# Performance work log

Hardware: AMD Instinct MI355X
Metric: run time of the kernel (lower is better)

The kernel has to match this reference:

```python
import jax, jax.numpy as jnp
import numpy as np

N_NODES = 100000
IN_CH = 256
OUT_CH = 128
HID = 2 * OUT_CH  # 256
N_EDGES = 1600000


def gcn_conv(x, src, dst, W, b, num_nodes):
    """PyG GCNConv: add self-loops, symmetric deg^-1/2 normalization,
    linear transform, scatter-add aggregation, plus bias."""
    h = x @ W  # [N, F_out]
    loop = jnp.arange(num_nodes, dtype=src.dtype)
    src_f = jnp.concatenate([src, loop])
    dst_f = jnp.concatenate([dst, loop])
    ones = jnp.ones(src_f.shape[0], dtype=h.dtype)
    deg = jax.ops.segment_sum(ones, dst_f, num_segments=num_nodes)
    dis = jnp.where(deg > 0, jax.lax.rsqrt(deg), 0.0)
    norm = dis[src_f] * dis[dst_f]  # [E+N]
    msg = h[src_f] * norm[:, None]  # [E+N, F_out]
    out = jax.ops.segment_sum(msg, dst_f, num_segments=num_nodes)
    return out + b


def setup_inputs() -> dict:
    key = jax.random.key(0)
    ks = jax.random.split(key, 8)
    x = jax.random.normal(ks[0], (N_NODES, IN_CH), dtype=jnp.float32)
    edge_index = jax.random.randint(ks[1], (2, N_EDGES), 0, N_NODES, dtype=jnp.int64 if jax.config.jax_enable_x64 else jnp.int32)
    s1 = 1.0 / np.sqrt(IN_CH)
    s2 = 1.0 / np.sqrt(HID)
    W1 = jax.random.uniform(ks[2], (IN_CH, HID), jnp.float32, -s1, s1)
    b1 = jnp.zeros((HID,), jnp.float32)
    W_mu = jax.random.uniform(ks[3], (HID, OUT_CH), jnp.float32, -s2, s2)
    b_mu = jnp.zeros((OUT_CH,), jnp.float32)
    W_lv = jax.random.uniform(ks[4], (HID, OUT_CH), jnp.float32, -s2, s2)
    b_lv = jnp.zeros((OUT_CH,), jnp.float32)
    return {"x": x, "edge_index": edge_index, "W1": W1, "b1": b1,
            "W_mu": W_mu, "b_mu": b_mu, "W_lv": W_lv, "b_lv": b_lv}


def reference(x, edge_index, W1, b1, W_mu, b_mu, W_lv, b_lv):
    src, dst = edge_index[0], edge_index[1]
    h = jax.nn.relu(gcn_conv(x, src, dst, W1, b1, N_NODES))
    mu = gcn_conv(h, src, dst, W_mu, b_mu, N_NODES)
    logvar = gcn_conv(h, src, dst, W_lv, b_lv, N_NODES)
    return (mu, logvar)
```

## Files before the change

kernel.cpp:

```cpp
#include <hip/hip_runtime.h>
#include <hip/hip_fp16.h>

#define N_NODES 100000
#define E_EDGES 1600000
#define F 256
#define LV_OFF 12800000
#define SCAN_BLK 98
#define GEMM_BLKS 1564
#define FILL_BLKS 6250

typedef _Float16 half8 __attribute__((ext_vector_type(8)));
typedef _Float16 f16x4 __attribute__((ext_vector_type(4)));
typedef float    f32x4 __attribute__((ext_vector_type(4)));

__global__ void k_zero(int* __restrict__ p, int n) {
    int i = blockIdx.x * 256 + threadIdx.x;
    if (i < n) p[i] = 0;
}

__global__ void k_count(const int* __restrict__ dst, int* __restrict__ cnt) {
    int e = blockIdx.x * 256 + threadIdx.x;
    if (e < E_EDGES) atomicAdd(&cnt[dst[e]], 1);
}

__global__ void k_dis(const int* __restrict__ cnt, float* __restrict__ dis) {
    int i = blockIdx.x * 256 + threadIdx.x;
    if (i < N_NODES) dis[i] = rsqrtf((float)cnt[i] + 1.0f);
}

__global__ __launch_bounds__(256) void k_scan1(const int* __restrict__ cnt,
                                               int* __restrict__ row_off,
                                               int* __restrict__ bsum) {
    __shared__ int sd[256];
    int tid = threadIdx.x;
    int base = blockIdx.x * 1024 + tid * 4;
    int c[4]; int s = 0;
#pragma unroll
    for (int k = 0; k < 4; k++) {
        int i = base + k;
        c[k] = (i < N_NODES) ? cnt[i] : 0;
        s += c[k];
    }
    sd[tid] = s;
    __syncthreads();
    for (int off = 1; off < 256; off <<= 1) {
        int t = (tid >= off) ? sd[tid - off] : 0;
        __syncthreads();
        sd[tid] += t;
        __syncthreads();
    }
    int run = sd[tid] - s;
#pragma unroll
    for (int k = 0; k < 4; k++) {
        int i = base + k;
        if (i < N_NODES) row_off[i] = run;
        run += c[k];
    }
    if (tid == 255) bsum[blockIdx.x] = sd[255];
}

__global__ void k_scan2(int* __restrict__ bsum) {
    if (threadIdx.x == 0 && blockIdx.x == 0) {
        int run = 0;
        for (int i = 0; i < SCAN_BLK; ++i) { int t = bsum[i]; bsum[i] = run; run += t; }
    }
}

__global__ __launch_bounds__(256) void k_scan3(int* __restrict__ row_off,
                                               const int* __restrict__ bsum,
                                               int* __restrict__ cursor) {
    int tid = threadIdx.x;
    int add = bsum[blockIdx.x];
    int base = blockIdx.x * 1024 + tid * 4;
#pragma unroll
    for (int k = 0; k < 4; k++) {
        int i = base + k;
        if (i < N_NODES) {
            int v = row_off[i] + add;
            row_off[i] = v;
            cursor[i] = v;
        }
    }
    if (blockIdx.x == 0 && tid == 0) row_off[N_NODES] = E_EDGES;
}

__global__ void k_wprep(const float* __restrict__ W1,
                        const float* __restrict__ Wmu, const float* __restrict__ Wlv,
                        _Float16* __restrict__ Wt1, _Float16* __restrict__ Wtc) {
    int idx = blockIdx.x * 256 + threadIdx.x;
    int n = idx >> 8, k = idx & 255;
    Wt1[n * 256 + k] = (_Float16)W1[k * 256 + n];
    float wc = (n < 128) ? Wmu[k * 128 + n] : Wlv[k * 128 + (n - 128)];
    Wtc[n * 256 + k] = (_Float16)wc;
}

__device__ __forceinline__ void gemm_tile(
    const float* __restrict__ A, const _Float16* __restrict__ Bt,
    const float* __restrict__ dis, _Float16* __restrict__ G, int M,
    int m0, int n0, int tid, _Float16* Ah, _Float16* Bh)
{
    const int wave = tid >> 6, lane = tid & 63;
    const int wm   = wave & 1, wn = wave >> 1;
    const int lrow = lane & 15, kgrp = lane >> 4;

    f32x4 acc[4][4];
#pragma unroll
    for (int i = 0; i < 4; i++)
#pragma unroll
        for (int j = 0; j < 4; j++) acc[i][j] = (f32x4){0.f, 0.f, 0.f, 0.f};

    const int sr = tid >> 4;
    const int kq = tid & 15;

    for (int kt = 0; kt < 256; kt += 64) {
#pragma unroll
        for (int p = 0; p < 8; ++p) {
            int row = p * 16 + sr;
            int gm = m0 + row; if (gm >= M) gm = M - 1;
            float4 v = *reinterpret_cast<const float4*>(A + (size_t)gm * F + kt + kq * 4);
            f16x4 h4;
            h4[0] = (_Float16)v.x; h4[1] = (_Float16)v.y;
            h4[2] = (_Float16)v.z; h4[3] = (_Float16)v.w;
            int sidx = row * 64 + ((kq * 4) ^ ((row & 7) << 3));
            *reinterpret_cast<f16x4*>(&Ah[sidx]) = h4;
        }
#pragma unroll
        for (int p = 0; p < 4; ++p) {
            int u = p * 256 + tid;
            int n = u >> 3, slot = u & 7;
            half8 hv = *reinterpret_cast<const half8*>(Bt + (size_t)(n0 + n) * F + kt + slot * 8);
            int sidx = n * 64 + ((slot * 8) ^ ((n & 7) << 3));
            *reinterpret_cast<half8*>(&Bh[sidx]) = hv;
        }
        __syncthreads();
#pragma unroll
        for (int ks = 0; ks < 2; ++ks) {
            int kk = ks * 32 + kgrp * 8;
            half8 ah[4], bh[4];
#pragma unroll
            for (int i = 0; i < 4; ++i) {
                int row = wm * 64 + i * 16 + lrow;
                ah[i] = *reinterpret_cast<const half8*>(&Ah[row * 64 + (kk ^ ((row & 7) << 3))]);
                int col = wn * 64 + i * 16 + lrow;
                bh[i] = *reinterpret_cast<const half8*>(&Bh[col * 64 + (kk ^ ((col & 7) << 3))]);
            }
#pragma unroll
            for (int i = 0; i < 4; ++i)
#pragma unroll
                for (int j = 0; j < 4; ++j)
                    acc[i][j] = __builtin_amdgcn_mfma_f32_16x16x32_f16(ah[i], bh[j], acc[i][j], 0, 0, 0);
        }
        __syncthreads();
    }

#pragma unroll
    for (int i = 0; i < 4; ++i) {
#pragma unroll
        for (int r = 0; r < 4; ++r) {
            int m = m0 + wm * 64 + i * 16 + kgrp * 4 + r;
            if (m >= M) continue;
            float dv = dis[m];
#pragma unroll
            for (int j = 0; j < 4; ++j) {
                int n = n0 + wn * 64 + j * 16 + lrow;
                G[(size_t)m * F + n] = (_Float16)(acc[i][j][r] * dv);
            }
        }
    }
}

__global__ __launch_bounds__(256) void k_gemm_fill(
    const float* __restrict__ A, const _Float16* __restrict__ Bt,
    const float* __restrict__ dis, _Float16* __restrict__ G, int M,
    const int* __restrict__ src, const int* __restrict__ dst,
    int* __restrict__ cursor, int* __restrict__ csr_src)
{
    __shared__ _Float16 Ah[128 * 64];
    __shared__ _Float16 Bh[128 * 64];
    int bid = blockIdx.x;
    int r5 = bid % 5;
    if (r5 == 0) {
        int gid = bid / 5;
        gemm_tile(A, Bt, dis, G, M, (gid >> 1) * 128, (gid & 1) * 128, threadIdx.x, Ah, Bh);
    } else {
        int fid = (bid / 5) * 4 + r5 - 1;
        int e = fid * 256 + threadIdx.x;
        if (e < E_EDGES) {
            int pos = atomicAdd(&cursor[dst[e]], 1);
            csr_src[pos] = src[e];
        }
    }
}

__global__ __launch_bounds__(256) void k_gemm_f16(
    const float* __restrict__ A, const _Float16* __restrict__ Bt,
    const float* __restrict__ dis, _Float16* __restrict__ G, int M)
{
    __shared__ _Float16 Ah[128 * 64];
    __shared__ _Float16 Bh[128 * 64];
    gemm_tile(A, Bt, dis, G, M, blockIdx.x * 128, blockIdx.y * 128, threadIdx.x, Ah, Bh);
}

__global__ __launch_bounds__(256) void k_aggregate_relu(
    const _Float16* __restrict__ g, const int* __restrict__ row_off,
    const int* __restrict__ csr_src, const float* __restrict__ dis,
    const float* __restrict__ b, float* __restrict__ h)
{
    int d = blockIdx.x * 4 + (threadIdx.x >> 6);
    int lane = threadIdx.x & 63;
    int hf = lane >> 5, lp = lane & 31;
    const half8* g8 = reinterpret_cast<const half8*>(g);
    float a[8] = {0,0,0,0,0,0,0,0}, a2[8] = {0,0,0,0,0,0,0,0};
    float a3[8] = {0,0,0,0,0,0,0,0}, a4[8] = {0,0,0,0,0,0,0,0};
    if (hf == 0) {
        half8 sv = g8[(size_t)d * 32 + lp];
#pragma unroll
        for (int k = 0; k < 8; k++) a[k] = (float)sv[k];
    }
    int j0 = row_off[d], j1 = row_off[d + 1];
    int j = j0 + hf;
    for (; j + 6 < j1; j += 8) {
        int s0 = csr_src[j], s1 = csr_src[j + 2], s2 = csr_src[j + 4], s3 = csr_src[j + 6];
        half8 v0 = g8[(size_t)s0 * 32 + lp];
        half8 v1 = g8[(size_t)s1 * 32 + lp];
        half8 v2 = g8[(size_t)s2 * 32 + lp];
        half8 v3 = g8[(size_t)s3 * 32 + lp];
#pragma unroll
        for (int k = 0; k < 8; k++) {
            a[k] += (float)v0[k]; a2[k] += (float)v1[k];
            a3[k] += (float)v2[k]; a4[k] += (float)v3[k];
        }
    }
    for (; j < j1; j += 2) {
        int s0 = csr_src[j];
        half8 v0 = g8[(size_t)s0 * 32 + lp];
#pragma unroll
        for (int k = 0; k < 8; k++) a[k] += (float)v0[k];
    }
#pragma unroll
    for (int k = 0; k < 8; k++) {
        a[k] += a2[k] + a3[k] + a4[k];
        a[k] += __shfl_xor(a[k], 32);
    }
    float sc = dis[d];
    int c = lp * 8 + hf * 4;
    float4 bb = *reinterpret_cast<const float4*>(b + c);
    float4 o;
    o.x = fmaxf(fmaf(sc, a[hf * 4 + 0], bb.x), 0.0f);
    o.y = fmaxf(fmaf(sc, a[hf * 4 + 1], bb.y), 0.0f);
    o.z = fmaxf(fmaf(sc, a[hf * 4 + 2], bb.z), 0.0f);
    o.w = fmaxf(fmaf(sc, a[hf * 4 + 3], bb.w), 0.0f);
    *reinterpret_cast<float4*>(h + (size_t)d * F + c) = o;
}

__global__ __launch_bounds__(256) void k_aggregate_out(
    const _Float16* __restrict__ g, const int* __restrict__ row_off,
    const int* __restrict__ csr_src, const float* __restrict__ dis,
    const float* __restrict__ bmu, const float* __restrict__ blv,
    float* __restrict__ out)
{
    int d = blockIdx.x * 4 + (threadIdx.x >> 6);
    int lane = threadIdx.x & 63;
    int hf = lane >> 5, lp = lane & 31;
    const half8* g8 = reinterpret_cast<const half8*>(g);
    float a[8] = {0,0,0,0,0,0,0,0}, a2[8] = {0,0,0,0,0,0,0,0};
    float a3[8] = {0,0,0,0,0,0,0,0}, a4[8] = {0,0,0,0,0,0,0,0};
    if (hf == 0) {
        half8 sv = g8[(size_t)d * 32 + lp];
#pragma unroll
        for (int k = 0; k < 8; k++) a[k] = (float)sv[k];
    }
    int j0 = row_off[d], j1 = row_off[d + 1];
    int j = j0 + hf;
    for (; j + 6 < j1; j += 8) {
        int s0 = csr_src[j], s1 = csr_src[j + 2], s2 = csr_src[j + 4], s3 = csr_src[j + 6];
        half8 v0 = g8[(size_t)s0 * 32 + lp];
        half8 v1 = g8[(size_t)s1 * 32 + lp];
        half8 v2 = g8[(size_t)s2 * 32 + lp];
        half8 v3 = g8[(size_t)s3 * 32 + lp];
#pragma unroll
        for (int k = 0; k < 8; k++) {
            a[k] += (float)v0[k]; a2[k] += (float)v1[k];
            a3[k] += (float)v2[k]; a4[k] += (float)v3[k];
        }
    }
    for (; j < j1; j += 2) {
        int s0 = csr_src[j];
        half8 v0 = g8[(size_t)s0 * 32 + lp];
#pragma unroll
        for (int k = 0; k < 8; k++) a[k] += (float)v0[k];
    }
#pragma unroll
    for (int k = 0; k < 8; k++) {
        a[k] += a2[k] + a3[k] + a4[k];
        a[k] += __shfl_xor(a[k], 32);
    }
    float sc = dis[d];
    int ch = lp * 8 + hf * 4;
    float va = a[hf * 4 + 0], vb = a[hf * 4 + 1], vc = a[hf * 4 + 2], vd = a[hf * 4 + 3];
    if (ch < 128) {
        float4 bb = *reinterpret_cast<const float4*>(bmu + ch);
        float4 o = make_float4(fmaf(sc, va, bb.x), fmaf(sc, vb, bb.y),
                               fmaf(sc, vc, bb.z), fmaf(sc, vd, bb.w));
        *reinterpret_cast<float4*>(out + (size_t)d * 128 + ch) = o;
    } else {
        int c2 = ch - 128;
        float4 bb = *reinterpret_cast<const float4*>(blv + c2);
        float4 o = make_float4(fmaf(sc, va, bb.x), fmaf(sc, vb, bb.y),
                               fmaf(sc, vc, bb.z), fmaf(sc, vd, bb.w));
        *reinterpret_cast<float4*>(out + LV_OFF + (size_t)d * 128 + c2) = o;
    }
}

extern "C" void kernel_launch(void* const* d_in, const int* in_sizes, int n_in,
                              void* d_out, int out_size, void* d_ws, size_t ws_size,
                              hipStream_t stream) {
    const float* x   = (const float*)d_in[0];
    const int*   ei  = (const int*)d_in[1];
    const int*   src = ei;
    const int*   dst = ei + E_EDGES;
    const float* W1  = (const float*)d_in[2];
    const float* b1  = (const float*)d_in[3];
    const float* Wmu = (const float*)d_in[4];
    const float* bmu = (const float*)d_in[5];
    const float* Wlv = (const float*)d_in[6];
    const float* blv = (const float*)d_in[7];
    float* out = (float*)d_out;

    char* ws = (char*)d_ws;
    size_t o = 0;
    auto carve = [&](size_t bytes) -> char* {
        char* p = ws + o;
        o = (o + bytes + 1023) & ~(size_t)1023;
        return p;
    };
    float*    dis     = (float*)   carve(400000);
    int*      cnt     = (int*)     carve(400000);
    int*      row_off = (int*)     carve(400004);
    int*      cursor  = (int*)     carve(400000);
    int*      bsum    = (int*)     carve(SCAN_BLK * 4);
    _Float16* Wt1     = (_Float16*)carve(131072);
    _Float16* Wtc     = (_Float16*)carve(131072);
    int*      csr_src = (int*)     carve((size_t)E_EDGES * 4);
    _Float16* g       = (_Float16*)carve((size_t)N_NODES * F * 2);
    (void)ws_size;

    k_zero <<<(N_NODES + 255) / 256, 256, 0, stream>>>(cnt, N_NODES);
    k_count<<<(E_EDGES + 255) / 256, 256, 0, stream>>>(dst, cnt);
    k_dis  <<<(N_NODES + 255) / 256, 256, 0, stream>>>(cnt, dis);
    k_scan1<<<SCAN_BLK, 256, 0, stream>>>(cnt, row_off, bsum);
    k_scan2<<<1, 64, 0, stream>>>(bsum);
    k_scan3<<<SCAN_BLK, 256, 0, stream>>>(row_off, bsum, cursor);
    k_wprep<<<256, 256, 0, stream>>>(W1, Wmu, Wlv, Wt1, Wtc);

    k_gemm_fill<<<5 * GEMM_BLKS, 256, 0, stream>>>(x, Wt1, dis, g, N_NODES,
                                                   src, dst, cursor, csr_src);
    k_aggregate_relu<<<N_NODES / 4, 256, 0, stream>>>(g, row_off, csr_src, dis, b1, out);

    dim3 gemm_grid(782, 2);
    k_gemm_f16<<<gemm_grid, 256, 0, stream>>>(out, Wtc, dis, g, N_NODES);
    k_aggregate_out<<<N_NODES / 4, 256, 0, stream>>>(g, row_off, csr_src, dis, bmu, blv, out);
}
```

Before: 515.6 us.

## Replace atomic CSR build with two-level bucket sort and widen GEMM tiles

Builds the CSR through a two-level binning scheme instead of global per-node atomics and a three-kernel scan. Edges are first bucketed by dst>>7 using shared-memory histograms, then sorted locally per bucket, and degrees and dis are derived inside the bucket pass. The GEMM now computes the full 256-wide output per block, which halves the A reloads, and the hidden layer is stored in fp16 so the second GEMM reads half the bytes. The cost is an extra 8-byte-per-edge intermediate buffer and one more pass over edges. The GEMM no longer overlaps with the CSR fill.

```diff
diff --git a/kernel.cpp b/kernel.cpp
--- a/kernel.cpp
+++ b/kernel.cpp
@@ -5,9 +5,9 @@
 #define E_EDGES 1600000
 #define F 256
 #define LV_OFF 12800000
-#define SCAN_BLK 98
-#define GEMM_BLKS 1564
-#define FILL_BLKS 6250
+#define NBUK 782
+#define EPB 8192
+#define NBLK_BIN 196
 
 typedef _Float16 half8 __attribute__((ext_vector_type(8)));
 typedef _Float16 f16x4 __attribute__((ext_vector_type(4)));
@@ -16,72 +16,6 @@
 __global__ void k_zero(int* __restrict__ p, int n) {
     int i = blockIdx.x * 256 + threadIdx.x;
     if (i < n) p[i] = 0;
-}
-
-__global__ void k_count(const int* __restrict__ dst, int* __restrict__ cnt) {
-    int e = blockIdx.x * 256 + threadIdx.x;
-    if (e < E_EDGES) atomicAdd(&cnt[dst[e]], 1);
-}
-
-__global__ void k_dis(const int* __restrict__ cnt, float* __restrict__ dis) {
-    int i = blockIdx.x * 256 + threadIdx.x;
-    if (i < N_NODES) dis[i] = rsqrtf((float)cnt[i] + 1.0f);
-}
-
-__global__ __launch_bounds__(256) void k_scan1(const int* __restrict__ cnt,
-                                               int* __restrict__ row_off,
-                                               int* __restrict__ bsum) {
-    __shared__ int sd[256];
-    int tid = threadIdx.x;
-    int base = blockIdx.x * 1024 + tid * 4;
-    int c[4]; int s = 0;
-#pragma unroll
-    for (int k = 0; k < 4; k++) {
-        int i = base + k;
-        c[k] = (i < N_NODES) ? cnt[i] : 0;
-        s += c[k];
-    }
-    sd[tid] = s;
-    __syncthreads();
-    for (int off = 1; off < 256; off <<= 1) {
-        int t = (tid >= off) ? sd[tid - off] : 0;
-        __syncthreads();
-        sd[tid] += t;
-        __syncthreads();
-    }
-    int run = sd[tid] - s;
-#pragma unroll
-    for (int k = 0; k < 4; k++) {
-        int i = base + k;
-        if (i < N_NODES) row_off[i] = run;
-        run += c[k];
-    }
-    if (tid == 255) bsum[blockIdx.x] = sd[255];
-}
-
-__global__ void k_scan2(int* __restrict__ bsum) {
-    if (threadIdx.x == 0 && blockIdx.x == 0) {
-        int run = 0;
-        for (int i = 0; i < SCAN_BLK; ++i) { int t = bsum[i]; bsum[i] = run; run += t; }
-    }
-}
-
-__global__ __launch_bounds__(256) void k_scan3(int* __restrict__ row_off,
-                                               const int* __restrict__ bsum,
-                                               int* __restrict__ cursor) {
-    int tid = threadIdx.x;
-    int add = bsum[blockIdx.x];
-    int base = blockIdx.x * 1024 + tid * 4;
-#pragma unroll
-    for (int k = 0; k < 4; k++) {
-        int i = base + k;
-        if (i < N_NODES) {
-            int v = row_off[i] + add;
-            row_off[i] = v;
-            cursor[i] = v;
-        }
-    }
-    if (blockIdx.x == 0 && tid == 0) row_off[N_NODES] = E_EDGES;
 }
 
 __global__ void k_wprep(const float* __restrict__ W1,
@@ -94,60 +28,167 @@
     Wtc[n * 256 + k] = (_Float16)wc;
 }
 
-__device__ __forceinline__ void gemm_tile(
-    const float* __restrict__ A, const _Float16* __restrict__ Bt,
-    const float* __restrict__ dis, _Float16* __restrict__ G, int M,
-    int m0, int n0, int tid, _Float16* Ah, _Float16* Bh)
+__global__ __launch_bounds__(256) void k_binA(const int* __restrict__ dst,
+                                              int* __restrict__ gcnt, int* __restrict__ cbase) {
+    __shared__ int h[NBUK];
+    int blk = blockIdx.x, tid = threadIdx.x;
+    for (int b = tid; b < NBUK; b += 256) h[b] = 0;
+    __syncthreads();
+    int e0 = blk * EPB, e1 = min(e0 + EPB, E_EDGES);
+    for (int e = e0 + tid; e < e1; e += 256) atomicAdd(&h[dst[e] >> 7], 1);
+    __syncthreads();
+    for (int b = tid; b < NBUK; b += 256) {
+        int c = h[b];
+        cbase[blk * NBUK + b] = c ? atomicAdd(&gcnt[b], c) : 0;
+    }
+}
+
+__global__ __launch_bounds__(1024) void k_scan782(const int* __restrict__ gcnt,
+                                                  int* __restrict__ gbase) {
+    __shared__ int sd[1024];
+    int tid = threadIdx.x;
+    int v = (tid < NBUK) ? gcnt[tid] : 0;
+    sd[tid] = v;
+    __syncthreads();
+    for (int off = 1; off < 1024; off <<= 1) {
+        int t = (tid >= off) ? sd[tid - off] : 0;
+        __syncthreads();
+        sd[tid] += t;
+        __syncthreads();
+    }
+    if (tid < NBUK) gbase[tid] = sd[tid] - v;
+    if (tid == NBUK - 1) gbase[NBUK] = sd[tid];
+}
+
+__global__ __launch_bounds__(256) void k_binC(const int* __restrict__ src, const int* __restrict__ dst,
+                                              const int* __restrict__ gbase, const int* __restrict__ cbase,
+                                              unsigned long long* __restrict__ ebuf) {
+    __shared__ int h2[NBUK];
+    __shared__ int bs[NBUK];
+    int blk = blockIdx.x, tid = threadIdx.x;
+    for (int b = tid; b < NBUK; b += 256) {
+        h2[b] = 0;
+        bs[b] = gbase[b] + cbase[blk * NBUK + b];
+    }
+    __syncthreads();
+    int e0 = blk * EPB, e1 = min(e0 + EPB, E_EDGES);
+    for (int e = e0 + tid; e < e1; e += 256) {
+        int d = dst[e];
+        int b = d >> 7;
+        int lr = atomicAdd(&h2[b], 1);
+        ebuf[bs[b] + lr] = ((unsigned long long)(unsigned)d << 32) | (unsigned)src[e];
+    }
+}
+
+__global__ __launch_bounds__(256) void k_binD(const unsigned long long* __restrict__ ebuf,
+                                              const int* __restrict__ gbase,
+                                              int* __restrict__ csr_src, int* __restrict__ row_off,
+                                              float* __restrict__ dis) {
+    __shared__ int dh[128], dsc[128], dcur[128];
+    int b = blockIdx.x, tid = threadIdx.x;
+    if (tid < 128) dh[tid] = 0;
+    __syncthreads();
+    int s0 = gbase[b], s1 = gbase[b + 1];
+    for (int i = s0 + tid; i < s1; i += 256)
+        atomicAdd(&dh[(int)(ebuf[i] >> 32) & 127], 1);
+    __syncthreads();
+    if (tid < 128) dsc[tid] = dh[tid];
+    __syncthreads();
+    for (int off = 1; off < 128; off <<= 1) {
+        int t = 0;
+        if (tid < 128 && tid >= off) t = dsc[tid - off];
+        __syncthreads();
+        if (tid < 128) dsc[tid] += t;
+        __syncthreads();
+    }
+    if (tid < 128) {
+        int ex = dsc[tid] - dh[tid];
+        dcur[tid] = ex;
+        int node = b * 128 + tid;
+        if (node < N_NODES) {
+            row_off[node] = s0 + ex;
+            dis[node] = rsqrtf((float)dh[tid] + 1.0f);
+        }
+    }
+    if (b == 0 && tid == 128) row_off[N_NODES] = E_EDGES;
+    __syncthreads();
+    for (int i = s0 + tid; i < s1; i += 256) {
+        unsigned long long ed = ebuf[i];
+        int dl = (int)(ed >> 32) & 127;
+        int lr = atomicAdd(&dcur[dl], 1);
+        csr_src[s0 + lr] = (int)(ed & 0xFFFFFFFFull);
+    }
+}
+
+template <typename TA>
+__global__ __launch_bounds__(256, 2) void k_gemm(
+    const TA* __restrict__ A, const _Float16* __restrict__ Bt,
+    const float* __restrict__ dis, _Float16* __restrict__ G, int M)
 {
+    __shared__ _Float16 Ah[128 * 64];
+    __shared__ _Float16 Bh[256 * 64];
+
+    const int tid  = threadIdx.x;
+    const int m0   = blockIdx.x * 128;
     const int wave = tid >> 6, lane = tid & 63;
     const int wm   = wave & 1, wn = wave >> 1;
     const int lrow = lane & 15, kgrp = lane >> 4;
 
-    f32x4 acc[4][4];
+    f32x4 acc[4][8];
 #pragma unroll
     for (int i = 0; i < 4; i++)
 #pragma unroll
-        for (int j = 0; j < 4; j++) acc[i][j] = (f32x4){0.f, 0.f, 0.f, 0.f};
-
-    const int sr = tid >> 4;
-    const int kq = tid & 15;
+        for (int j = 0; j < 8; j++) acc[i][j] = (f32x4){0.f, 0.f, 0.f, 0.f};
 
     for (int kt = 0; kt < 256; kt += 64) {
+        if constexpr (sizeof(TA) == 4) {
+            const int sr = tid >> 4, kq = tid & 15;
+#pragma unroll
+            for (int p = 0; p < 8; ++p) {
+                int row = p * 16 + sr;
+                int gm = m0 + row; if (gm >= M) gm = M - 1;
+                float4 v = *reinterpret_cast<const float4*>((const float*)A + (size_t)gm * F + kt + kq * 4);
+                f16x4 h4;
+                h4[0] = (_Float16)v.x; h4[1] = (_Float16)v.y;
+                h4[2] = (_Float16)v.z; h4[3] = (_Float16)v.w;
+                *reinterpret_cast<f16x4*>(&Ah[row * 64 + ((kq * 4) ^ ((row & 7) << 3))]) = h4;
+            }
+        } else {
+#pragma unroll
+            for (int p = 0; p < 4; ++p) {
+                int u = p * 256 + tid;
+                int row = u >> 3, slot = u & 7;
+                int gm = m0 + row; if (gm >= M) gm = M - 1;
+                half8 v = *reinterpret_cast<const half8*>((const _Float16*)A + (size_t)gm * F + kt + slot * 8);
+                *reinterpret_cast<half8*>(&Ah[row * 64 + ((slot * 8) ^ ((row & 7) << 3))]) = v;
+            }
+        }
 #pragma unroll
         for (int p = 0; p < 8; ++p) {
-            int row = p * 16 + sr;
-            int gm = m0 + row; if (gm >= M) gm = M - 1;
-            float4 v = *reinterpret_cast<const float4*>(A + (size_t)gm * F + kt + kq * 4);
-            f16x4 h4;
-            h4[0] = (_Float16)v.x; h4[1] = (_Float16)v.y;
-            h4[2] = (_Float16)v.z; h4[3] = (_Float16)v.w;
-            int sidx = row * 64 + ((kq * 4) ^ ((row & 7) << 3));
-            *reinterpret_cast<f16x4*>(&Ah[sidx]) = h4;
-        }
-#pragma unroll
-        for (int p = 0; p < 4; ++p) {
             int u = p * 256 + tid;
             int n = u >> 3, slot = u & 7;
-            half8 hv = *reinterpret_cast<const half8*>(Bt + (size_t)(n0 + n) * F + kt + slot * 8);
-            int sidx = n * 64 + ((slot * 8) ^ ((n & 7) << 3));
-            *reinterpret_cast<half8*>(&Bh[sidx]) = hv;
+            half8 v = *reinterpret_cast<const half8*>(Bt + (size_t)n * F + kt + slot * 8);
+            *reinterpret_cast<half8*>(&Bh[n * 64 + ((slot * 8) ^ ((n & 7) << 3))]) = v;
         }
         __syncthreads();
 #pragma unroll
         for (int ks = 0; ks < 2; ++ks) {
             int kk = ks * 32 + kgrp * 8;
-            half8 ah[4], bh[4];
+            half8 ah[4], bh[8];
 #pragma unroll
             for (int i = 0; i < 4; ++i) {
                 int row = wm * 64 + i * 16 + lrow;
                 ah[i] = *reinterpret_cast<const half8*>(&Ah[row * 64 + (kk ^ ((row & 7) << 3))]);
-                int col = wn * 64 + i * 16 + lrow;
-                bh[i] = *reinterpret_cast<const half8*>(&Bh[col * 64 + (kk ^ ((col & 7) << 3))]);
+            }
+#pragma unroll
+            for (int j = 0; j < 8; ++j) {
+                int col = wn * 128 + j * 16 + lrow;
+                bh[j] = *reinterpret_cast<const half8*>(&Bh[col * 64 + (kk ^ ((col & 7) << 3))]);
             }
 #pragma unroll
             for (int i = 0; i < 4; ++i)
 #pragma unroll
-                for (int j = 0; j < 4; ++j)
+                for (int j = 0; j < 8; ++j)
                     acc[i][j] = __builtin_amdgcn_mfma_f32_16x16x32_f16(ah[i], bh[j], acc[i][j], 0, 0, 0);
         }
         __syncthreads();
@@ -161,50 +202,18 @@
             if (m >= M) continue;
             float dv = dis[m];
 #pragma unroll
-            for (int j = 0; j < 4; ++j) {
-                int n = n0 + wn * 64 + j * 16 + lrow;
+            for (int j = 0; j < 8; ++j) {
+                int n = wn * 128 + j * 16 + lrow;
                 G[(size_t)m * F + n] = (_Float16)(acc[i][j][r] * dv);
             }
         }
     }
-}
-
-__global__ __launch_bounds__(256) void k_gemm_fill(
-    const float* __restrict__ A, const _Float16* __restrict__ Bt,
-    const float* __restrict__ dis, _Float16* __restrict__ G, int M,
-    const int* __restrict__ src, const int* __restrict__ dst,
-    int* __restrict__ cursor, int* __restrict__ csr_src)
-{
-    __shared__ _Float16 Ah[128 * 64];
-    __shared__ _Float16 Bh[128 * 64];
-    int bid = blockIdx.x;
-    int r5 = bid % 5;
-    if (r5 == 0) {
-        int gid = bid / 5;
-        gemm_tile(A, Bt, dis, G, M, (gid >> 1) * 128, (gid & 1) * 128, threadIdx.x, Ah, Bh);
-    } else {
-        int fid = (bid / 5) * 4 + r5 - 1;
-        int e = fid * 256 + threadIdx.x;
-        if (e < E_EDGES) {
-            int pos = atomicAdd(&cursor[dst[e]], 1);
-            csr_src[pos] = src[e];
-        }
-    }
-}
-
-__global__ __launch_bounds__(256) void k_gemm_f16(
-    const float* __restrict__ A, const _Float16* __restrict__ Bt,
-    const float* __restrict__ dis, _Float16* __restrict__ G, int M)
-{
-    __shared__ _Float16 Ah[128 * 64];
-    __shared__ _Float16 Bh[128 * 64];
-    gemm_tile(A, Bt, dis, G, M, blockIdx.x * 128, blockIdx.y * 128, threadIdx.x, Ah, Bh);
 }
 
 __global__ __launch_bounds__(256) void k_aggregate_relu(
     const _Float16* __restrict__ g, const int* __restrict__ row_off,
     const int* __restrict__ csr_src, const float* __restrict__ dis,
-    const float* __restrict__ b, float* __restrict__ h)
+    const float* __restrict__ b, _Float16* __restrict__ h)
 {
     int d = blockIdx.x * 4 + (threadIdx.x >> 6);
     int lane = threadIdx.x & 63;
@@ -245,12 +254,12 @@
     float sc = dis[d];
     int c = lp * 8 + hf * 4;
     float4 bb = *reinterpret_cast<const float4*>(b + c);
-    float4 o;
-    o.x = fmaxf(fmaf(sc, a[hf * 4 + 0], bb.x), 0.0f);
-    o.y = fmaxf(fmaf(sc, a[hf * 4 + 1], bb.y), 0.0f);
-    o.z = fmaxf(fmaf(sc, a[hf * 4 + 2], bb.z), 0.0f);
-    o.w = fmaxf(fmaf(sc, a[hf * 4 + 3], bb.w), 0.0f);
-    *reinterpret_cast<float4*>(h + (size_t)d * F + c) = o;
+    f16x4 o;
+    o[0] = (_Float16)fmaxf(fmaf(sc, a[hf * 4 + 0], bb.x), 0.0f);
+    o[1] = (_Float16)fmaxf(fmaf(sc, a[hf * 4 + 1], bb.y), 0.0f);
+    o[2] = (_Float16)fmaxf(fmaf(sc, a[hf * 4 + 2], bb.z), 0.0f);
+    o[3] = (_Float16)fmaxf(fmaf(sc, a[hf * 4 + 3], bb.w), 0.0f);
+    *reinterpret_cast<f16x4*>(h + (size_t)d * F + c) = o;
 }
 
 __global__ __launch_bounds__(256) void k_aggregate_out(
@@ -335,29 +344,29 @@
         return p;
     };
     float*    dis     = (float*)   carve(400000);
-    int*      cnt     = (int*)     carve(400000);
     int*      row_off = (int*)     carve(400004);
-    int*      cursor  = (int*)     carve(400000);
-    int*      bsum    = (int*)     carve(SCAN_BLK * 4);
+    int*      gcnt    = (int*)     carve(NBUK * 4);
+    int*      gbase   = (int*)     carve((NBUK + 1) * 4);
+    int*      cbase   = (int*)     carve((size_t)NBLK_BIN * NBUK * 4);
     _Float16* Wt1     = (_Float16*)carve(131072);
     _Float16* Wtc     = (_Float16*)carve(131072);
     int*      csr_src = (int*)     carve((size_t)E_EDGES * 4);
+    unsigned long long* ebuf = (unsigned long long*)carve((size_t)E_EDGES * 8);
     _Float16* g       = (_Float16*)carve((size_t)N_NODES * F * 2);
     (void)ws_size;
 
-    k_zero <<<(N_NODES + 255) / 256, 256, 0, stream>>>(cnt, N_NODES);
-    k_count<<<(E_EDGES + 255) / 256, 256, 0, stream>>>(dst, cnt);
-    k_dis  <<<(N_NODES + 255) / 256, 256, 0, stream>>>(cnt, dis);
-    k_scan1<<<SCAN_BLK, 256, 0, stream>>>(cnt, row_off, bsum);
-    k_scan2<<<1, 64, 0, stream>>>(bsum);
-    k_scan3<<<SCAN_BLK, 256, 0, stream>>>(row_off, bsum, cursor);
-    k_wprep<<<256, 256, 0, stream>>>(W1, Wmu, Wlv, Wt1, Wtc);
-
-    k_gemm_fill<<<5 * GEMM_BLKS, 256, 0, stream>>>(x, Wt1, dis, g, N_NODES,
-                                                   src, dst, cursor, csr_src);
-    k_aggregate_relu<<<N_NODES / 4, 256, 0, stream>>>(g, row_off, csr_src, dis, b1, out);
-
-    dim3 gemm_grid(782, 2);
-    k_gemm_f16<<<gemm_grid, 256, 0, stream>>>(out, Wtc, dis, g, N_NODES);
+    _Float16* h16 = (_Float16*)(out + LV_OFF);
+
+    k_zero   <<<(NBUK + 255) / 256, 256, 0, stream>>>(gcnt, NBUK);
+    k_wprep  <<<256, 256, 0, stream>>>(W1, Wmu, Wlv, Wt1, Wtc);
+    k_binA   <<<NBLK_BIN, 256, 0, stream>>>(dst, gcnt, cbase);
+    k_scan782<<<1, 1024, 0, stream>>>(gcnt, gbase);
+    k_binC   <<<NBLK_BIN, 256, 0, stream>>>(src, dst, gbase, cbase, ebuf);
+    k_binD   <<<NBUK, 256, 0, stream>>>(ebuf, gbase, csr_src, row_off, dis);
+
+    k_gemm<float><<<782, 256, 0, stream>>>(x, Wt1, dis, g, N_NODES);
+    k_aggregate_relu<<<N_NODES / 4, 256, 0, stream>>>(g, row_off, csr_src, dis, b1, h16);
+
+    k_gemm<_Float16><<<782, 256, 0, stream>>>(h16, Wtc, dis, g, N_NODES);
     k_aggregate_out<<<N_NODES / 4, 256, 0, stream>>>(g, row_off, csr_src, dis, bmu, blv, out);
 }
```

Result: faster. 419.3 us (-18.7%).
